# Performance work log

Measured on AMD Instinct MI355X. Metric: run time of the kernel, lower is better.

The kernel has to match this reference:

```python
import jax, jax.numpy as jnp
import numpy as np

B = 4
N_TOTAL = 40000
N_SRC0, N_DST0, E0 = 30000, 15000, 360000
N_DST1, E1 = 7500, 180000
D_IN, OUT = 64, 32
H1, C1 = 8, 8
H2, C2 = 1, OUT
NEG_SLOPE = 0.2


def setup_inputs() -> dict:
    key = jax.random.key(0)
    ks = jax.random.split(key, 16)
    inp = {
        'x': jax.random.normal(ks[0], (B, N_TOTAL, D_IN), dtype=jnp.float32),
        'n_id0': jax.random.randint(ks[1], (N_SRC0,), 0, N_SRC0),
        'res_n_id0': jax.random.randint(ks[2], (N_DST0,), 0, N_SRC0),
        'edge_src0': jax.random.randint(ks[3], (E0,), 0, N_SRC0),
        'edge_dst0': jax.random.randint(ks[4], (E0,), 0, N_DST0),
        'res_n_id1': jax.random.randint(ks[5], (N_DST1,), 0, N_DST0),
        'edge_src1': jax.random.randint(ks[6], (E1,), 0, N_DST0),
        'edge_dst1': jax.random.randint(ks[7], (E1,), 0, N_DST1),
        # GATConv params (Glorot-ish scale)
        'W1': jax.random.normal(ks[8], (D_IN, H1 * C1), dtype=jnp.float32) / np.sqrt(D_IN),
        'att_src1': jax.random.normal(ks[9], (H1, C1), dtype=jnp.float32) / np.sqrt(C1),
        'att_dst1': jax.random.normal(ks[10], (H1, C1), dtype=jnp.float32) / np.sqrt(C1),
        'b1': jnp.zeros((H1 * C1,), dtype=jnp.float32),
        'W2': jax.random.normal(ks[11], (H1 * C1, H2 * C2), dtype=jnp.float32) / np.sqrt(H1 * C1),
        'att_src2': jax.random.normal(ks[12], (H2, C2), dtype=jnp.float32) / np.sqrt(C2),
        'att_dst2': jax.random.normal(ks[13], (H2, C2), dtype=jnp.float32) / np.sqrt(C2),
        'b2': jnp.zeros((H2 * C2,), dtype=jnp.float32),
    }
    return inp


def gat_conv(x_src, x_dst, src, dst, W, a_src, a_dst, bias, n_dst, H, C):
    """Bipartite PyG-style GATConv (concat=True, eval mode, no self-loops)."""
    b = x_src.shape[0]
    hs = (x_src @ W).reshape(b, -1, H, C)            # [B, Ns, H, C]
    hd = (x_dst @ W).reshape(b, -1, H, C)            # [B, Nd, H, C]
    es = jnp.einsum('bnhc,hc->bnh', hs, a_src)       # [B, Ns, H]
    ed = jnp.einsum('bnhc,hc->bnh', hd, a_dst)       # [B, Nd, H]
    e = jax.nn.leaky_relu(es[:, src] + ed[:, dst], NEG_SLOPE)  # [B, E, H]
    eT = jnp.swapaxes(e, 0, 1)                       # [E, B, H] (segment over axis 0)
    m = jax.ops.segment_max(eT, dst, num_segments=n_dst)
    p = jnp.exp(eT - m[dst])
    den = jax.ops.segment_sum(p, dst, num_segments=n_dst)
    alpha = p / den[dst]                             # [E, B, H]
    msg = alpha[..., None] * jnp.swapaxes(hs[:, src], 0, 1)    # [E, B, H, C]
    out = jax.ops.segment_sum(msg, dst, num_segments=n_dst)    # [Nd, B, H, C]
    out = jnp.swapaxes(out, 0, 1).reshape(b, n_dst, H * C)
    return out + bias


def reference(x, n_id0, res_n_id0, edge_src0, edge_dst0, res_n_id1, edge_src1,
              edge_dst1, W1, att_src1, att_dst1, b1, W2, att_src2, att_dst2, b2):
    xt = x[:, n_id0, :]                                        # [B, N_SRC0, D_IN]
    h = gat_conv(xt, xt[:, res_n_id0, :], edge_src0, edge_dst0,
                 W1, att_src1, att_dst1, b1, N_DST0, H1, C1)
    h = jax.nn.elu(h)                                          # dropout = identity (eval)
    out = gat_conv(h, h[:, res_n_id1, :], edge_src1, edge_dst1,
                   W2, att_src2, att_dst2, b2, N_DST1, H2, C2)
    return out                                                 # [B, N_DST1, OUT]
```

## Files before the change

### kernel.cpp

```cpp
#include <hip/hip_runtime.h>

#define NB 4
#define NT 40000
#define NS0 30000
#define ND0 15000
#define NE0 360000
#define ND1 7500
#define NE1 180000
#define NEG 0.2f

#define CAP 64
#define K1B ((NB*NS0)/64)
#define SB8 ((NE0 + NE1 + 2047)/2048)

#define BKT(p) ((((p) & 7) << 3) | ((p) >> 3))

typedef __attribute__((ext_vector_type(8))) short bf8;
typedef __attribute__((ext_vector_type(4))) float f4;
typedef __attribute__((ext_vector_type(2))) float f2;

__device__ __forceinline__ unsigned short f2bf(float f) {
    unsigned u = __float_as_uint(f);
    u += 0x7FFF + ((u >> 16) & 1);
    return (unsigned short)(u >> 16);
}
__device__ __forceinline__ f2 upk(unsigned u) {
    f2 r;
    r.x = __uint_as_float(u << 16);
    r.y = __uint_as_float(u & 0xFFFF0000u);
    return r;
}

__global__ __launch_bounds__(256) void kA_gemm_scat(
        const float* __restrict__ x, const int* __restrict__ n_id0,
        const float* __restrict__ W1, const float* __restrict__ a_src,
        const float* __restrict__ a_dst,
        unsigned short* __restrict__ ht1b, float* __restrict__ es1, float* __restrict__ ed1,
        const int* __restrict__ esrc0, const int* __restrict__ edst0,
        const int* __restrict__ esrc1, const int* __restrict__ edst1,
        int* __restrict__ cur0, int* __restrict__ cur1,
        int* __restrict__ srcsort0, int* __restrict__ srcsort1) {
    __shared__ unsigned short xtb[64*72];
    __shared__ unsigned short wtb[64*72];
    __shared__ float asl[64], adl[64];
    if (blockIdx.x >= K1B) {
        int base = (blockIdx.x - K1B) * 2048 + threadIdx.x;
        #pragma unroll
        for (int p = 0; p < 8; ++p) {
            int t = base + p * 256;
            if (t < NE0) {
                int d = edst0[t];
                int pos = atomicAdd(&cur0[d], 1);
                if (pos < CAP) srcsort0[d*CAP + BKT(pos)] = esrc0[t];
            } else if (t < NE0 + NE1) {
                int e = t - NE0;
                int d = edst1[e];
                int pos = atomicAdd(&cur1[d], 1);
                if (pos < CAP) srcsort1[d*CAP + BKT(pos)] = esrc1[e];
            }
        }
        return;
    }
    int bid = blockIdx.x;
    int t = threadIdx.x;
    int r   = t >> 2;
    int sub = t & 3;
    int row_s = bid * 64 + r;
    int bs = row_s / NS0;
    int ns = row_s - bs * NS0;
    const float* xrow = x + ((size_t)(bs * NT + n_id0[ns])) * 64;
    float4 xv0 = *(const float4*)&xrow[(sub +  0) * 4];
    float4 xv1 = *(const float4*)&xrow[(sub +  4) * 4];
    float4 xv2 = *(const float4*)&xrow[(sub +  8) * 4];
    float4 xv3 = *(const float4*)&xrow[(sub + 12) * 4];
    {
        int k = t >> 2, nb = (t & 3) * 16;
        const float* wrow = &W1[k*64 + nb];
        #pragma unroll
        for (int j = 0; j < 16; j += 4) {
            float4 v = *(const float4*)&wrow[j];
            wtb[(nb+j+0)*72 + k] = f2bf(v.x);
            wtb[(nb+j+1)*72 + k] = f2bf(v.y);
            wtb[(nb+j+2)*72 + k] = f2bf(v.z);
            wtb[(nb+j+3)*72 + k] = f2bf(v.w);
        }
    }
    if (t < 64) { asl[t] = a_src[t]; adl[t] = a_dst[t]; }
    {
        ushort4 u;
        u.x = f2bf(xv0.x); u.y = f2bf(xv0.y); u.z = f2bf(xv0.z); u.w = f2bf(xv0.w);
        *(ushort4*)&xtb[r*72 + (sub +  0) * 4] = u;
        u.x = f2bf(xv1.x); u.y = f2bf(xv1.y); u.z = f2bf(xv1.z); u.w = f2bf(xv1.w);
        *(ushort4*)&xtb[r*72 + (sub +  4) * 4] = u;
        u.x = f2bf(xv2.x); u.y = f2bf(xv2.y); u.z = f2bf(xv2.z); u.w = f2bf(xv2.w);
        *(ushort4*)&xtb[r*72 + (sub +  8) * 4] = u;
        u.x = f2bf(xv3.x); u.y = f2bf(xv3.y); u.z = f2bf(xv3.z); u.w = f2bf(xv3.w);
        *(ushort4*)&xtb[r*72 + (sub + 12) * 4] = u;
    }
    __syncthreads();
    int w = t >> 6, lane = t & 63, quad = lane >> 4, cl = lane & 15;
    int arow = 16*w + cl;
    bf8 a0 = *(const bf8*)&xtb[arow*72 + quad*8];
    bf8 a1 = *(const bf8*)&xtb[arow*72 + 32 + quad*8];
    f4 acc[4];
    #pragma unroll
    for (int sub2 = 0; sub2 < 4; ++sub2) {
        int n = sub2*16 + cl;
        bf8 b0 = *(const bf8*)&wtb[n*72 + quad*8];
        bf8 b1v = *(const bf8*)&wtb[n*72 + 32 + quad*8];
        f4 c = {0.f, 0.f, 0.f, 0.f};
        c = __builtin_amdgcn_mfma_f32_16x16x32_bf16(a0, b0, c, 0, 0, 0);
        c = __builtin_amdgcn_mfma_f32_16x16x32_bf16(a1, b1v, c, 0, 0, 0);
        acc[sub2] = c;
    }
    __syncthreads();
    unsigned short* ob = xtb;
    #pragma unroll
    for (int sub2 = 0; sub2 < 4; ++sub2)
        #pragma unroll
        for (int rr = 0; rr < 4; ++rr)
            ob[(16*w + 4*quad + rr)*64 + sub2*16 + cl] = f2bf(acc[sub2][rr]);
    int rbase = bid*64 + 16*w + quad*4;
    #pragma unroll
    for (int rr = 0; rr < 4; ++rr) {
        #pragma unroll
        for (int sub2 = 0; sub2 < 4; ++sub2) {
            int col = sub2*16 + cl;
            float ps = acc[sub2][rr] * asl[col];
            float pd = acc[sub2][rr] * adl[col];
            ps += __shfl_xor(ps, 1); ps += __shfl_xor(ps, 2); ps += __shfl_xor(ps, 4);
            pd += __shfl_xor(pd, 1); pd += __shfl_xor(pd, 2); pd += __shfl_xor(pd, 4);
            if ((cl & 7) == 0) {
                int h = sub2*2 + (cl >> 3);
                es1[(rbase + rr)*8 + h] = ps;
                ed1[(rbase + rr)*8 + h] = pd;
            }
        }
    }
    __syncthreads();
    {
        int row = t >> 3;
        int c8  = t & 7;
        #pragma unroll
        for (int rep = 0; rep < 2; ++rep) {
            int rr2 = row + rep*32;
            uint4 v = *(const uint4*)&ob[rr2*64 + c8*8];
            *(uint4*)&ht1b[((size_t)(bid*64 + rr2))*64 + c8*8] = v;
        }
    }
}

__global__ __launch_bounds__(256) void k3_agg1_node2(
        const int* __restrict__ srcsort0, const int* __restrict__ cur0,
        const int* __restrict__ res0,
        const float* __restrict__ es1, const float* __restrict__ ed1,
        const unsigned short* __restrict__ ht1b, const float* __restrict__ b1,
        const float* __restrict__ W2, const float* __restrict__ a_src2,
        const float* __restrict__ a_dst2,
        float* __restrict__ ht2, float* __restrict__ es2, float* __restrict__ ed2) {
    __shared__ float W2t[32][68];
    __shared__ float as2[32], ad2[32];
    __shared__ float b1l[64];
    __shared__ float hsh[4][64];
    int t = threadIdx.x;
    {
        float4 v0 = *(const float4*)&W2[t*8];
        float4 v1 = *(const float4*)&W2[t*8 + 4];
        int k = t >> 2, c = (t & 3) * 8;
        W2t[c+0][k] = v0.x; W2t[c+1][k] = v0.y; W2t[c+2][k] = v0.z; W2t[c+3][k] = v0.w;
        W2t[c+4][k] = v1.x; W2t[c+5][k] = v1.y; W2t[c+6][k] = v1.z; W2t[c+7][k] = v1.w;
    }
    if (t < 32) { as2[t] = a_src2[t]; ad2[t] = a_dst2[t]; }
    if (t < 64) b1l[t] = b1[t];
    __syncthreads();
    int xcd = blockIdx.x & 7;
    int b = xcd >> 1;
    int chunk = (blockIdx.x >> 3) * 2 + (xcd & 1);
    int wv = t >> 6;
    int d = chunk * 4 + wv;
    int lane = t & 63;
    int grp = lane >> 3;
    int c = lane & 7;
    int dn = res0[d];
    float edv = ed1[(b*NS0 + dn)*8 + c];
    int start = d * CAP;
    int cnt = min(cur0[d], CAP);
    const float* esb = es1 + (size_t)b*NS0*8;
    const unsigned short* htb = ht1b + (size_t)b*NS0*64;
    f2 a01 = {0.f, 0.f}, a23 = {0.f, 0.f}, a45 = {0.f, 0.f}, a67 = {0.f, 0.f};
    float wsum = 0.f;
    int i = grp;
    int pp = start + grp*8;
    int4 sv = *(const int4*)&srcsort0[pp];
    bool v0 = i      < cnt, v1 = i + 8  < cnt,
         v2 = i + 16 < cnt, v3 = i + 24 < cnt;
    int s0 = v0 ? sv.x : 0;
    int s1 = v1 ? sv.y : 0;
    int s2 = v2 ? sv.z : 0;
    int s3 = v3 ? sv.w : 0;
    for (;;) {
        float e0 = esb[s0*8 + c], e1 = esb[s1*8 + c];
        float e2 = esb[s2*8 + c], e3 = esb[s3*8 + c];
        uint4 h0 = *(const uint4*)&htb[(size_t)s0*64 + c*8];
        uint4 h1 = *(const uint4*)&htb[(size_t)s1*64 + c*8];
        uint4 h2 = *(const uint4*)&htb[(size_t)s2*64 + c*8];
        uint4 h3 = *(const uint4*)&htb[(size_t)s3*64 + c*8];
        int ni = i + 32;
        bool nv0 = false, nv1 = false, nv2 = false, nv3 = false;
        int t0 = 0, t1 = 0, t2 = 0, t3 = 0;
        if (ni < cnt) {
            int4 nsv = *(const int4*)&srcsort0[pp + 4];
            nv0 = true;            nv1 = ni + 8  < cnt;
            nv2 = ni + 16 < cnt;   nv3 = ni + 24 < cnt;
            t0 =       nsv.x;
            t1 = nv1 ? nsv.y : 0;
            t2 = nv2 ? nsv.z : 0;
            t3 = nv3 ? nsv.w : 0;
        }
        e0 += edv; e1 += edv; e2 += edv; e3 += edv;
        e0 = e0 > 0.f ? e0 : NEG * e0;
        e1 = e1 > 0.f ? e1 : NEG * e1;
        e2 = e2 > 0.f ? e2 : NEG * e2;
        e3 = e3 > 0.f ? e3 : NEG * e3;
        float w0 = v0 ? __expf(e0) : 0.f;
        float w1 = v1 ? __expf(e1) : 0.f;
        float w2 = v2 ? __expf(e2) : 0.f;
        float w3 = v3 ? __expf(e3) : 0.f;
        a01 += w0 * upk(h0.x); a23 += w0 * upk(h0.y);
        a45 += w0 * upk(h0.z); a67 += w0 * upk(h0.w);
        a01 += w1 * upk(h1.x); a23 += w1 * upk(h1.y);
        a45 += w1 * upk(h1.z); a67 += w1 * upk(h1.w);
        a01 += w2 * upk(h2.x); a23 += w2 * upk(h2.y);
        a45 += w2 * upk(h2.z); a67 += w2 * upk(h2.w);
        a01 += w3 * upk(h3.x); a23 += w3 * upk(h3.y);
        a45 += w3 * upk(h3.z); a67 += w3 * upk(h3.w);
        wsum += (w0 + w1) + (w2 + w3);
        i = ni; pp += 4;
        s0 = t0; s1 = t1; s2 = t2; s3 = t3;
        v0 = nv0; v1 = nv1; v2 = nv2; v3 = nv3;
        if (i >= cnt) break;
    }
    float acc[8] = {a01.x, a01.y, a23.x, a23.y, a45.x, a45.y, a67.x, a67.y};
    int g0 = grp & 1, g1 = (grp >> 1) & 1, g2 = grp >> 2;
    float n0, n1, n2, n3;
    {
        float s, r;
        s = g0 ? acc[0] : acc[1]; r = __shfl_xor(s, 8);  n0 = (g0 ? acc[1] : acc[0]) + r;
        s = g0 ? acc[2] : acc[3]; r = __shfl_xor(s, 8);  n1 = (g0 ? acc[3] : acc[2]) + r;
        s = g0 ? acc[4] : acc[5]; r = __shfl_xor(s, 8);  n2 = (g0 ? acc[5] : acc[4]) + r;
        s = g0 ? acc[6] : acc[7]; r = __shfl_xor(s, 8);  n3 = (g0 ? acc[7] : acc[6]) + r;
    }
    float m0, m1;
    {
        float s, r;
        s = g1 ? n0 : n1; r = __shfl_xor(s, 16); m0 = (g1 ? n1 : n0) + r;
        s = g1 ? n2 : n3; r = __shfl_xor(s, 16); m1 = (g1 ? n3 : n2) + r;
    }
    float fin;
    {
        float s = g2 ? m0 : m1; float r = __shfl_xor(s, 32); fin = (g2 ? m1 : m0) + r;
    }
    wsum += __shfl_xor(wsum, 8); wsum += __shfl_xor(wsum, 16); wsum += __shfl_xor(wsum, 32);
    float inv = cnt > 0 ? 1.f / wsum : 0.f;
    float o = fin * inv + b1l[(c << 3) | grp];
    o = o > 0.f ? o : __expf(o) - 1.f;
    hsh[wv][(c << 3) | grp] = o;
    int c2 = lane & 31, half = lane >> 5;
    const float4* hp = (const float4*)&hsh[wv][half * 32];
    const float4* wp = (const float4*)&W2t[c2][half * 32];
    float acc2 = 0.f;
    #pragma unroll
    for (int q = 0; q < 8; ++q) {
        float4 hv = hp[q];
        float4 w4 = wp[q];
        acc2 = fmaf(hv.x, w4.x, acc2); acc2 = fmaf(hv.y, w4.y, acc2);
        acc2 = fmaf(hv.z, w4.z, acc2); acc2 = fmaf(hv.w, w4.w, acc2);
    }
    acc2 += __shfl_xor(acc2, 32);
    float ps = acc2 * as2[c2];
    float pd = acc2 * ad2[c2];
    ps += __shfl_xor(ps, 1); ps += __shfl_xor(ps, 2); ps += __shfl_xor(ps, 4);
    ps += __shfl_xor(ps, 8); ps += __shfl_xor(ps, 16);
    pd += __shfl_xor(pd, 1); pd += __shfl_xor(pd, 2); pd += __shfl_xor(pd, 4);
    pd += __shfl_xor(pd, 8); pd += __shfl_xor(pd, 16);
    int row = b*ND0 + d;
    if (half == 0) ht2[(size_t)row*32 + c2] = acc2;
    if (lane == 0) { es2[row] = ps; ed2[row] = pd; }
}

__global__ __launch_bounds__(256) void k7_agg2(
        const int* __restrict__ srcsort1, const int* __restrict__ cur1,
        const int* __restrict__ res1,
        const float* __restrict__ es2, const float* __restrict__ ed2,
        const float* __restrict__ ht2, const float* __restrict__ b2,
        float* __restrict__ outp) {
    int xcd = blockIdx.x & 7;
    int b = xcd >> 1;
    int chunk = (blockIdx.x >> 3) * 2 + (xcd & 1);
    if (chunk >= ND1/4) return;
    int d = chunk * 4 + (threadIdx.x >> 6);
    int lane = threadIdx.x & 63;
    int grp = lane >> 3;
    int c = lane & 7;
    int dn = res1[d];
    float edv = ed2[b*ND0 + dn];
    int start = d * CAP;
    int cnt = min(cur1[d], CAP);
    const float* esb = es2 + (size_t)b*ND0;
    const float* htb = ht2 + (size_t)b*ND0*32;
    f4 accv = {0.f, 0.f, 0.f, 0.f};
    float wsum = 0.f;
    int i = grp;
    int pp = start + grp*8;
    int4 sv = *(const int4*)&srcsort1[pp];
    bool v0 = i      < cnt, v1 = i + 8  < cnt,
         v2 = i + 16 < cnt, v3 = i + 24 < cnt;
    int s0 = v0 ? sv.x : 0;
    int s1 = v1 ? sv.y : 0;
    int s2 = v2 ? sv.z : 0;
    int s3 = v3 ? sv.w : 0;
    for (;;) {
        float lg0 = esb[s0], lg1 = esb[s1], lg2 = esb[s2], lg3 = esb[s3];
        f4 h0 = *(const f4*)&htb[(size_t)s0*32 + c*4];
        f4 h1 = *(const f4*)&htb[(size_t)s1*32 + c*4];
        f4 h2 = *(const f4*)&htb[(size_t)s2*32 + c*4];
        f4 h3 = *(const f4*)&htb[(size_t)s3*32 + c*4];
        int ni = i + 32;
        bool nv0 = false, nv1 = false, nv2 = false, nv3 = false;
        int t0 = 0, t1 = 0, t2 = 0, t3 = 0;
        if (ni < cnt) {
            int4 nsv = *(const int4*)&srcsort1[pp + 4];
            nv0 = true;            nv1 = ni + 8  < cnt;
            nv2 = ni + 16 < cnt;   nv3 = ni + 24 < cnt;
            t0 =       nsv.x;
            t1 = nv1 ? nsv.y : 0;
            t2 = nv2 ? nsv.z : 0;
            t3 = nv3 ? nsv.w : 0;
        }
        lg0 += edv; lg1 += edv; lg2 += edv; lg3 += edv;
        lg0 = lg0 > 0.f ? lg0 : NEG * lg0;
        lg1 = lg1 > 0.f ? lg1 : NEG * lg1;
        lg2 = lg2 > 0.f ? lg2 : NEG * lg2;
        lg3 = lg3 > 0.f ? lg3 : NEG * lg3;
        float w0 = v0 ? __expf(lg0) : 0.f;
        float w1 = v1 ? __expf(lg1) : 0.f;
        float w2 = v2 ? __expf(lg2) : 0.f;
        float w3 = v3 ? __expf(lg3) : 0.f;
        accv += w0 * h0;
        accv += w1 * h1;
        accv += w2 * h2;
        accv += w3 * h3;
        wsum += (w0 + w1) + (w2 + w3);
        i = ni; pp += 4;
        s0 = t0; s1 = t1; s2 = t2; s3 = t3;
        v0 = nv0; v1 = nv1; v2 = nv2; v3 = nv3;
        if (i >= cnt) break;
    }
    float ax = accv.x, ay = accv.y, az = accv.z, aw = accv.w;
    ax += __shfl_xor(ax, 8); ax += __shfl_xor(ax, 16); ax += __shfl_xor(ax, 32);
    ay += __shfl_xor(ay, 8); ay += __shfl_xor(ay, 16); ay += __shfl_xor(ay, 32);
    az += __shfl_xor(az, 8); az += __shfl_xor(az, 16); az += __shfl_xor(az, 32);
    aw += __shfl_xor(aw, 8); aw += __shfl_xor(aw, 16); aw += __shfl_xor(aw, 32);
    wsum += __shfl_xor(wsum, 8); wsum += __shfl_xor(wsum, 16); wsum += __shfl_xor(wsum, 32);
    if (grp == 0) {
        float inv = cnt > 0 ? 1.f / wsum : 0.f;
        float4 bb = *(const float4*)&b2[c*4];
        float4 o;
        o.x = ax*inv + bb.x; o.y = ay*inv + bb.y;
        o.z = az*inv + bb.z; o.w = aw*inv + bb.w;
        *(float4*)&outp[((size_t)(b*ND1 + d))*32 + c*4] = o;
    }
}

extern "C" void kernel_launch(void* const* d_in, const int* in_sizes, int n_in,
                              void* d_out, int out_size, void* d_ws, size_t ws_size,
                              hipStream_t stream) {
    const float* x        = (const float*)d_in[0];
    const int*   n_id0    = (const int*)d_in[1];
    const int*   res0     = (const int*)d_in[2];
    const int*   esrc0    = (const int*)d_in[3];
    const int*   edst0    = (const int*)d_in[4];
    const int*   res1     = (const int*)d_in[5];
    const int*   esrc1    = (const int*)d_in[6];
    const int*   edst1    = (const int*)d_in[7];
    const float* W1       = (const float*)d_in[8];
    const float* a_src1   = (const float*)d_in[9];
    const float* a_dst1   = (const float*)d_in[10];
    const float* b1       = (const float*)d_in[11];
    const float* W2       = (const float*)d_in[12];
    const float* a_src2   = (const float*)d_in[13];
    const float* a_dst2   = (const float*)d_in[14];
    const float* b2       = (const float*)d_in[15];
    float* outp = (float*)d_out;

    char* base = (char*)d_ws;
    unsigned short* ht1b = (unsigned short*)base;
    float* es1  = (float*)(base + 15360000);
    float* ed1  = es1 + 960000;
    float* ht2  = ed1 + 960000;
    float* es2  = ht2 + 1920000;
    float* ed2  = es2 + 60000;
    int* cur0     = (int*)(ed2 + 60000);
    int* cur1     = cur0 + ND0;
    int* srcsort0 = cur1 + ND1;
    int* srcsort1 = srcsort0 + ND0*CAP;

    hipMemsetAsync(cur0, 0, (ND0 + ND1) * sizeof(int), stream);
    kA_gemm_scat<<<K1B + SB8, 256, 0, stream>>>(x, n_id0, W1, a_src1, a_dst1,
                                                ht1b, es1, ed1,
                                                esrc0, edst0, esrc1, edst1,
                                                cur0, cur1, srcsort0, srcsort1);
    k3_agg1_node2<<<NB*(ND0/4), 256, 0, stream>>>(srcsort0, cur0, res0, es1, ed1, ht1b, b1,
                                                  W2, a_src2, a_dst2, ht2, es2, ed2);
    k7_agg2<<<7504, 256, 0, stream>>>(srcsort1, cur1, res1, es2, ed2, ht2, b2, outp);
}
```

Baseline: 183.6 us.

## Store bucketed edge sources as 16-bit indices and use one edge per scatter thread

The per-destination source-index buckets are narrowed from 32-bit to 16-bit, since all source indices fit under 65536. This halves the bytes for the scatter writes and for the index loads in both aggregation kernels, which now read ushort4 instead of int4. The scatter blocks also drop from 8 edges per thread to 1 edge per thread, launching about eight times as many small blocks to spread the atomics across more waves. The risk is that the narrower 8-byte index loads and the extra block-launch overhead offset the bandwidth saved.

```diff
diff --git a/kernel.cpp b/kernel.cpp
--- a/kernel.cpp
+++ b/kernel.cpp
@@ -11,7 +11,7 @@
 
 #define CAP 64
 #define K1B ((NB*NS0)/64)
-#define SB8 ((NE0 + NE1 + 2047)/2048)
+#define SB1 ((NE0 + NE1 + 255)/256)
 
 #define BKT(p) ((((p) & 7) << 3) | ((p) >> 3))
 
@@ -39,25 +39,21 @@
         const int* __restrict__ esrc0, const int* __restrict__ edst0,
         const int* __restrict__ esrc1, const int* __restrict__ edst1,
         int* __restrict__ cur0, int* __restrict__ cur1,
-        int* __restrict__ srcsort0, int* __restrict__ srcsort1) {
+        unsigned short* __restrict__ srcsort0, unsigned short* __restrict__ srcsort1) {
     __shared__ unsigned short xtb[64*72];
     __shared__ unsigned short wtb[64*72];
     __shared__ float asl[64], adl[64];
     if (blockIdx.x >= K1B) {
-        int base = (blockIdx.x - K1B) * 2048 + threadIdx.x;
-        #pragma unroll
-        for (int p = 0; p < 8; ++p) {
-            int t = base + p * 256;
-            if (t < NE0) {
-                int d = edst0[t];
-                int pos = atomicAdd(&cur0[d], 1);
-                if (pos < CAP) srcsort0[d*CAP + BKT(pos)] = esrc0[t];
-            } else if (t < NE0 + NE1) {
-                int e = t - NE0;
-                int d = edst1[e];
-                int pos = atomicAdd(&cur1[d], 1);
-                if (pos < CAP) srcsort1[d*CAP + BKT(pos)] = esrc1[e];
-            }
+        int t = (blockIdx.x - K1B) * 256 + threadIdx.x;
+        if (t < NE0) {
+            int d = edst0[t];
+            int pos = atomicAdd(&cur0[d], 1);
+            if (pos < CAP) srcsort0[d*CAP + BKT(pos)] = (unsigned short)esrc0[t];
+        } else if (t < NE0 + NE1) {
+            int e = t - NE0;
+            int d = edst1[e];
+            int pos = atomicAdd(&cur1[d], 1);
+            if (pos < CAP) srcsort1[d*CAP + BKT(pos)] = (unsigned short)esrc1[e];
         }
         return;
     }
@@ -151,7 +147,7 @@
 }
 
 __global__ __launch_bounds__(256) void k3_agg1_node2(
-        const int* __restrict__ srcsort0, const int* __restrict__ cur0,
+        const unsigned short* __restrict__ srcsort0, const int* __restrict__ cur0,
         const int* __restrict__ res0,
         const float* __restrict__ es1, const float* __restrict__ ed1,
         const unsigned short* __restrict__ ht1b, const float* __restrict__ b1,
@@ -191,13 +187,13 @@
     float wsum = 0.f;
     int i = grp;
     int pp = start + grp*8;
-    int4 sv = *(const int4*)&srcsort0[pp];
+    ushort4 sv = *(const ushort4*)&srcsort0[pp];
     bool v0 = i      < cnt, v1 = i + 8  < cnt,
          v2 = i + 16 < cnt, v3 = i + 24 < cnt;
-    int s0 = v0 ? sv.x : 0;
-    int s1 = v1 ? sv.y : 0;
-    int s2 = v2 ? sv.z : 0;
-    int s3 = v3 ? sv.w : 0;
+    int s0 = v0 ? (int)sv.x : 0;
+    int s1 = v1 ? (int)sv.y : 0;
+    int s2 = v2 ? (int)sv.z : 0;
+    int s3 = v3 ? (int)sv.w : 0;
     for (;;) {
         float e0 = esb[s0*8 + c], e1 = esb[s1*8 + c];
         float e2 = esb[s2*8 + c], e3 = esb[s3*8 + c];
@@ -209,13 +205,13 @@
         bool nv0 = false, nv1 = false, nv2 = false, nv3 = false;
         int t0 = 0, t1 = 0, t2 = 0, t3 = 0;
         if (ni < cnt) {
-            int4 nsv = *(const int4*)&srcsort0[pp + 4];
+            ushort4 nsv = *(const ushort4*)&srcsort0[pp + 4];
             nv0 = true;            nv1 = ni + 8  < cnt;
             nv2 = ni + 16 < cnt;   nv3 = ni + 24 < cnt;
-            t0 =       nsv.x;
-            t1 = nv1 ? nsv.y : 0;
-            t2 = nv2 ? nsv.z : 0;
-            t3 = nv3 ? nsv.w : 0;
+            t0 =       (int)nsv.x;
+            t1 = nv1 ? (int)nsv.y : 0;
+            t2 = nv2 ? (int)nsv.z : 0;
+            t3 = nv3 ? (int)nsv.w : 0;
         }
         e0 += edv; e1 += edv; e2 += edv; e3 += edv;
         e0 = e0 > 0.f ? e0 : NEG * e0;
@@ -289,7 +285,7 @@
 }
 
 __global__ __launch_bounds__(256) void k7_agg2(
-        const int* __restrict__ srcsort1, const int* __restrict__ cur1,
+        const unsigned short* __restrict__ srcsort1, const int* __restrict__ cur1,
         const int* __restrict__ res1,
         const float* __restrict__ es2, const float* __restrict__ ed2,
         const float* __restrict__ ht2, const float* __restrict__ b2,
@@ -312,13 +308,13 @@
     float wsum = 0.f;
     int i = grp;
     int pp = start + grp*8;
-    int4 sv = *(const int4*)&srcsort1[pp];
+    ushort4 sv = *(const ushort4*)&srcsort1[pp];
     bool v0 = i      < cnt, v1 = i + 8  < cnt,
          v2 = i + 16 < cnt, v3 = i + 24 < cnt;
-    int s0 = v0 ? sv.x : 0;
-    int s1 = v1 ? sv.y : 0;
-    int s2 = v2 ? sv.z : 0;
-    int s3 = v3 ? sv.w : 0;
+    int s0 = v0 ? (int)sv.x : 0;
+    int s1 = v1 ? (int)sv.y : 0;
+    int s2 = v2 ? (int)sv.z : 0;
+    int s3 = v3 ? (int)sv.w : 0;
     for (;;) {
         float lg0 = esb[s0], lg1 = esb[s1], lg2 = esb[s2], lg3 = esb[s3];
         f4 h0 = *(const f4*)&htb[(size_t)s0*32 + c*4];
@@ -329,13 +325,13 @@
         bool nv0 = false, nv1 = false, nv2 = false, nv3 = false;
         int t0 = 0, t1 = 0, t2 = 0, t3 = 0;
         if (ni < cnt) {
-            int4 nsv = *(const int4*)&srcsort1[pp + 4];
+            ushort4 nsv = *(const ushort4*)&srcsort1[pp + 4];
             nv0 = true;            nv1 = ni + 8  < cnt;
             nv2 = ni + 16 < cnt;   nv3 = ni + 24 < cnt;
-            t0 =       nsv.x;
-            t1 = nv1 ? nsv.y : 0;
-            t2 = nv2 ? nsv.z : 0;
-            t3 = nv3 ? nsv.w : 0;
+            t0 =       (int)nsv.x;
+            t1 = nv1 ? (int)nsv.y : 0;
+            t2 = nv2 ? (int)nsv.z : 0;
+            t3 = nv3 ? (int)nsv.w : 0;
         }
         lg0 += edv; lg1 += edv; lg2 += edv; lg3 += edv;
         lg0 = lg0 > 0.f ? lg0 : NEG * lg0;
@@ -402,11 +398,11 @@
     float* ed2  = es2 + 60000;
     int* cur0     = (int*)(ed2 + 60000);
     int* cur1     = cur0 + ND0;
-    int* srcsort0 = cur1 + ND1;
-    int* srcsort1 = srcsort0 + ND0*CAP;
+    unsigned short* srcsort0 = (unsigned short*)(cur1 + ND1);
+    unsigned short* srcsort1 = srcsort0 + ND0*CAP;
 
     hipMemsetAsync(cur0, 0, (ND0 + ND1) * sizeof(int), stream);
-    kA_gemm_scat<<<K1B + SB8, 256, 0, stream>>>(x, n_id0, W1, a_src1, a_dst1,
+    kA_gemm_scat<<<K1B + SB1, 256, 0, stream>>>(x, n_id0, W1, a_src1, a_dst1,
                                                 ht1b, es1, ed1,
                                                 esrc0, edst0, esrc1, edst1,
                                                 cur0, cur1, srcsort0, srcsort1);
```

Result: slower. 191.8 us (+4.5%).
